# Kernel optimization log

Measured on AMD Instinct MI355X. Metric: run time of the kernel, lower is better.

The kernel has to match this reference:

```python
import jax, jax.numpy as jnp
import numpy as np

N, D = 8192, 64

def setup_inputs() -> dict:
    key = jax.random.key(0)
    sentence = jax.random.uniform(key, (N, D), dtype=jnp.float32)
    return {"sentence": sentence}

def reference(sentence):
    # weights[i, j] = <sentence[i], sentence[j]>  -> [n, n]
    weights = jnp.einsum('id,jd->ij', sentence, sentence)
    # sum-normalize each row (NOT softmax)
    weights = weights / jnp.sum(weights, axis=1, keepdims=True)
    # reweighted vectors: [n, n] @ [n, d] -> [n, d]
    return jnp.matmul(weights, sentence)
```

## Files before the change

### kernel.cpp

```cpp
#include <hip/hip_runtime.h>

#define N 8192
#define D 64

__global__ __launch_bounds__(256) void gram_kernel(const float* __restrict__ S,
                                                   float* __restrict__ G,
                                                   float* __restrict__ t) {
    __shared__ float rows[4][D];
    const int tid = threadIdx.x;
    const int d = tid & 63;
    const int q = tid >> 6;

    float acc[16];
#pragma unroll
    for (int m = 0; m < 16; ++m) acc[m] = 0.f;
    float tacc = 0.f;

    const int rows_per_block = N / gridDim.x;
    const int row0 = blockIdx.x * rows_per_block;

    for (int j = row0; j < row0 + rows_per_block; j += 4) {
        rows[q][d] = S[(size_t)j * D + tid];
        __syncthreads();
#pragma unroll
        for (int r = 0; r < 4; ++r) {
            const float sd = rows[r][d];
            if (q == 0) tacc += sd;
#pragma unroll
            for (int m = 0; m < 16; ++m)
                acc[m] += rows[r][q * 16 + m] * sd;
        }
        __syncthreads();
    }

#pragma unroll
    for (int m = 0; m < 16; ++m)
        atomicAdd(&G[(q * 16 + m) * D + d], acc[m]);
    if (q == 0) atomicAdd(&t[d], tacc);
}

__global__ __launch_bounds__(256) void apply_kernel(const float* __restrict__ S,
                                                    const float* __restrict__ G,
                                                    const float* __restrict__ t,
                                                    float* __restrict__ out) {
    __shared__ float Gs[D * D];
    __shared__ float ts[D];
    const int tid = threadIdx.x;
    for (int i = tid; i < D * D; i += 256) Gs[i] = G[i];
    if (tid < D) ts[tid] = t[tid];
    __syncthreads();

    const int lane = tid & 63;
    const int wave = tid >> 6;
    const int nwaves = gridDim.x * 4;

    for (int i = blockIdx.x * 4 + wave; i < N; i += nwaves) {
        const float v = S[(size_t)i * D + lane];
        float accv = 0.f;
        float rs = 0.f;
#pragma unroll
        for (int k = 0; k < D; ++k) {
            const float sk = __shfl(v, k, 64);
            accv += sk * Gs[k * D + lane];
            rs += sk * ts[k];
        }
        out[(size_t)i * D + lane] = accv / rs;
    }
}

extern "C" void kernel_launch(void* const* d_in, const int* in_sizes, int n_in,
                              void* d_out, int out_size, void* d_ws, size_t ws_size,
                              hipStream_t stream) {
    const float* S = (const float*)d_in[0];
    float* out = (float*)d_out;
    float* G = (float*)d_ws;
    float* t = G + D * D;

    hipMemsetAsync(d_ws, 0, (D * D + D) * sizeof(float), stream);
    gram_kernel<<<64, 256, 0, stream>>>(S, G, t);
    apply_kernel<<<256, 256, 0, stream>>>(S, G, t, out);
}
```

Baseline: 84.72 us.

## Register-tile Gram accumulation and process two rows per wave in apply

The Gram kernel drops its shared-memory staging and barriers. Each thread now loads float4 slices of each row straight from global memory and accumulates a 4x4 register tile of the outer product, with the grid doubled to 128 blocks. The apply kernel uses float4 loads for G, gets each row sum with a butterfly shuffle reduction, and handles two rows per wave so each shared-memory G read feeds two FMAs. The apply grid grows to 512 blocks with a fixed four rows per wave. The tradeoff is redundant global loads across threads and more atomics per block in the Gram phase.

```diff
diff --git a/kernel.cpp b/kernel.cpp
--- a/kernel.cpp
+++ b/kernel.cpp
@@ -2,41 +2,53 @@
 
 #define N 8192
 #define D 64
+#define GRAM_BLOCKS 128
+#define APPLY_BLOCKS 512
 
 __global__ __launch_bounds__(256) void gram_kernel(const float* __restrict__ S,
                                                    float* __restrict__ G,
                                                    float* __restrict__ t) {
-    __shared__ float rows[4][D];
     const int tid = threadIdx.x;
-    const int d = tid & 63;
-    const int q = tid >> 6;
+    const int ty = tid >> 4;
+    const int tx = tid & 15;
 
-    float acc[16];
+    float acc[4][4];
 #pragma unroll
-    for (int m = 0; m < 16; ++m) acc[m] = 0.f;
-    float tacc = 0.f;
+    for (int i = 0; i < 4; ++i)
+#pragma unroll
+        for (int j = 0; j < 4; ++j) acc[i][j] = 0.f;
+    float tac[4] = {0.f, 0.f, 0.f, 0.f};
 
-    const int rows_per_block = N / gridDim.x;
-    const int row0 = blockIdx.x * rows_per_block;
+    const int rpb = N / GRAM_BLOCKS;
+    const int r0 = blockIdx.x * rpb;
+    const float* Sa = S + (size_t)r0 * D + 4 * ty;
+    const float* Sb = S + (size_t)r0 * D + 4 * tx;
 
-    for (int j = row0; j < row0 + rows_per_block; j += 4) {
-        rows[q][d] = S[(size_t)j * D + tid];
-        __syncthreads();
+#pragma unroll 4
+    for (int r = 0; r < rpb; ++r) {
+        const float4 a = *(const float4*)(Sa + (size_t)r * D);
+        const float4 b = *(const float4*)(Sb + (size_t)r * D);
+        const float av[4] = {a.x, a.y, a.z, a.w};
+        const float bv[4] = {b.x, b.y, b.z, b.w};
 #pragma unroll
-        for (int r = 0; r < 4; ++r) {
-            const float sd = rows[r][d];
-            if (q == 0) tacc += sd;
+        for (int i = 0; i < 4; ++i)
 #pragma unroll
-            for (int m = 0; m < 16; ++m)
-                acc[m] += rows[r][q * 16 + m] * sd;
+            for (int j = 0; j < 4; ++j) acc[i][j] += av[i] * bv[j];
+        if (ty == 0) {
+#pragma unroll
+            for (int j = 0; j < 4; ++j) tac[j] += bv[j];
         }
-        __syncthreads();
     }
 
 #pragma unroll
-    for (int m = 0; m < 16; ++m)
-        atomicAdd(&G[(q * 16 + m) * D + d], acc[m]);
-    if (q == 0) atomicAdd(&t[d], tacc);
+    for (int i = 0; i < 4; ++i)
+#pragma unroll
+        for (int j = 0; j < 4; ++j)
+            atomicAdd(&G[(4 * ty + i) * D + 4 * tx + j], acc[i][j]);
+    if (ty == 0) {
+#pragma unroll
+        for (int j = 0; j < 4; ++j) atomicAdd(&t[4 * tx + j], tac[j]);
+    }
 }
 
 __global__ __launch_bounds__(256) void apply_kernel(const float* __restrict__ S,
@@ -46,25 +58,40 @@
     __shared__ float Gs[D * D];
     __shared__ float ts[D];
     const int tid = threadIdx.x;
-    for (int i = tid; i < D * D; i += 256) Gs[i] = G[i];
+#pragma unroll
+    for (int i = tid; i < (D * D) / 4; i += 256)
+        ((float4*)Gs)[i] = ((const float4*)G)[i];
     if (tid < D) ts[tid] = t[tid];
     __syncthreads();
 
     const int lane = tid & 63;
-    const int wave = tid >> 6;
-    const int nwaves = gridDim.x * 4;
+    const int wid = tid >> 6;
+    const float tl = ts[lane];
+    const int i0 = (blockIdx.x * 4 + wid) * 4;
 
-    for (int i = blockIdx.x * 4 + wave; i < N; i += nwaves) {
-        const float v = S[(size_t)i * D + lane];
-        float accv = 0.f;
-        float rs = 0.f;
+#pragma unroll
+    for (int p = 0; p < 2; ++p) {
+        const int ia = i0 + 2 * p;
+        const int ib = ia + 1;
+        const float va = S[(size_t)ia * D + lane];
+        const float vb = S[(size_t)ib * D + lane];
+
+        float pa = va * tl, pb = vb * tl;
+#pragma unroll
+        for (int s = 1; s < 64; s <<= 1) {
+            pa += __shfl_xor(pa, s, 64);
+            pb += __shfl_xor(pb, s, 64);
+        }
+
+        float aa = 0.f, ab = 0.f;
 #pragma unroll
         for (int k = 0; k < D; ++k) {
-            const float sk = __shfl(v, k, 64);
-            accv += sk * Gs[k * D + lane];
-            rs += sk * ts[k];
+            const float g = Gs[k * D + lane];
+            aa += __shfl(va, k, 64) * g;
+            ab += __shfl(vb, k, 64) * g;
         }
-        out[(size_t)i * D + lane] = accv / rs;
+        out[(size_t)ia * D + lane] = aa / pa;
+        out[(size_t)ib * D + lane] = ab / pb;
     }
 }
 
@@ -77,6 +104,6 @@
     float* t = G + D * D;
 
     hipMemsetAsync(d_ws, 0, (D * D + D) * sizeof(float), stream);
-    gram_kernel<<<64, 256, 0, stream>>>(S, G, t);
-    apply_kernel<<<256, 256, 0, stream>>>(S, G, t, out);
+    gram_kernel<<<GRAM_BLOCKS, 256, 0, stream>>>(S, G, t);
+    apply_kernel<<<APPLY_BLOCKS, 256, 0, stream>>>(S, G, t, out);
 }
```

After: 89.17 us. 1.05x slower.
